# Optimization experiments

Measured on AMD Instinct MI355X. Metric: run time of the kernel, lower is better.

The kernel has to match this reference:

```python
import jax, jax.numpy as jnp
import numpy as np
import math

B, L = 32, 1000
N_CHAR, EMB, D_MODEL, N_HEADS, PRED_HS, N_OUT = 256, 512, 512, 8, 512, 8
D_HEAD = D_MODEL // N_HEADS


def _pos_encoding(seq_len, d_model, dtype=jnp.float32):
    pos = jnp.arange(seq_len, dtype=dtype)[:, None]                      # [L,1]
    div = jnp.exp(jnp.arange(0, d_model, 2, dtype=dtype) * (-math.log(10000.0) / d_model))
    pe = jnp.zeros((seq_len, d_model), dtype=dtype)
    pe = pe.at[:, 0::2].set(jnp.sin(pos * div))
    pe = pe.at[:, 1::2].set(jnp.cos(pos * div))
    return pe                                                            # [L,D]


def setup_inputs() -> dict:
    key = jax.random.key(0)
    ks = jax.random.split(key, 12)
    def xavier(k, shape):
        fan_in, fan_out = shape[1], shape[0]
        lim = math.sqrt(6.0 / (fan_in + fan_out))
        return jax.random.uniform(k, shape, jnp.float32, -lim, lim)
    data = jax.random.randint(ks[0], (B, L), 0, N_CHAR, dtype=jnp.int64)
    lengths = jnp.clip(jax.random.randint(ks[1], (B,), 0, L, dtype=jnp.int64), 1, L)
    emb = jax.random.normal(ks[2], (N_CHAR, EMB), jnp.float32) * math.sqrt(2.0 / (N_CHAR + EMB))
    return {
        'data': data,
        'lengths': lengths,
        'emb': emb,
        'Wq': xavier(ks[3], (D_MODEL, EMB)), 'bq': jnp.zeros((D_MODEL,), jnp.float32),
        'Wk': xavier(ks[4], (D_MODEL, EMB)), 'bk': jnp.zeros((D_MODEL,), jnp.float32),
        'Wv': xavier(ks[5], (D_MODEL, EMB)), 'bv': jnp.zeros((D_MODEL,), jnp.float32),
        'W1': xavier(ks[6], (PRED_HS, D_MODEL)), 'b1': jnp.full((PRED_HS,), 0.01, jnp.float32),
        'W2': xavier(ks[7], (N_OUT, PRED_HS)), 'b2': jnp.full((N_OUT,), 0.01, jnp.float32),
    }


def reference(data, lengths, emb, Wq, bq, Wk, bk, Wv, bv, W1, b1, W2, b2):
    bs, seq = data.shape
    x = emb[data]                                              # [B,L,E]
    x = x + _pos_encoding(seq, x.shape[-1], x.dtype)[None]     # positional encoding
    # q/k/v projections -> [B,L,H,dh]
    q = (x @ Wq.T + bq).reshape(bs, seq, N_HEADS, D_HEAD)
    k = (x @ Wk.T + bk).reshape(bs, seq, N_HEADS, D_HEAD)
    v = (x @ Wv.T + bv).reshape(bs, seq, N_HEADS, D_HEAD)
    scale = 1.0 / math.sqrt(D_HEAD)
    score = jnp.einsum('bqhd,bkhd->bhqk', q, k) * scale        # [B,H,L,L]
    causal = jnp.tril(jnp.ones((seq, seq), dtype=bool))        # True = keep
    score = jnp.where(causal[None, None], score, -jnp.inf)
    attn = jax.nn.softmax(score, axis=-1)
    ctx = jnp.einsum('bhqk,bkhd->bqhd', attn, v).reshape(bs, seq, D_MODEL)
    # take hidden state at last valid position per sequence
    ctx_last = jnp.take_along_axis(ctx, (lengths - 1)[:, None, None].astype(jnp.int32), axis=1)[:, 0]  # [B,D]
    h = jax.nn.leaky_relu(ctx_last @ W1.T + b1)                # pred layer 1
    out = jax.nn.relu(h @ W2.T + b2)                           # [B,8]
    out = jnp.mean(out, axis=-1)                               # [B]
    return jax.nn.leaky_relu(out)
```

## Files before the change

kernel.cpp:

```cpp
#include <hip/hip_runtime.h>
#include <math.h>

#define BATCH   32
#define LSEQ    1000
#define NHEADS  8
#define DHEAD   64
#define CHUNK   64
#define NCHUNK  16
#define PE_C    (-9.210340371976184f / 512.0f)

__device__ __forceinline__ float pe_val(int j, int e) {
  int ef = e & ~1;
  float dv  = __expf((float)ef * PE_C);
  float arg = (float)j * dv;
  return (e & 1) ? __cosf(arg) : __sinf(arg);
}

__global__ __launch_bounds__(256) void qfold_kernel(
    const int* __restrict__ data, const int* __restrict__ lengths,
    const float* __restrict__ emb,
    const float* __restrict__ Wq, const float* __restrict__ bq,
    const float* __restrict__ Wk, const float* __restrict__ bk,
    float* __restrict__ wfT4, float* __restrict__ bias_dot) {
  int h = blockIdx.x, b = blockIdx.y;
  int p = lengths[b] - 1;
  int t = threadIdx.x;
  __shared__ float xs[512];
  __shared__ float red[256];
  __shared__ float qs[64];
  int tok = data[b * LSEQ + p];
  const float* er = emb + (size_t)tok * 512;
  xs[t]       = er[t]       + pe_val(p, t);
  xs[t + 256] = er[t + 256] + pe_val(p, t + 256);
  __syncthreads();
  int col = h * 64 + (t & 63);
  int kp  = t >> 6;
  {
    const float* wr = Wq + (size_t)col * 512 + kp * 128;
    const float* xp = xs + kp * 128;
    float a = 0.0f;
    for (int e = 0; e < 128; e += 4) {
      float4 wv = *(const float4*)(wr + e);
      a += wv.x * xp[e] + wv.y * xp[e + 1] + wv.z * xp[e + 2] + wv.w * xp[e + 3];
    }
    red[t] = a;
  }
  __syncthreads();
  if (t < 64) {
    float qval = (red[t] + red[t + 64] + red[t + 128] + red[t + 192]
                  + bq[h * 64 + t]) * 0.125f;
    qs[t] = qval;
    float bd = qval * bk[h * 64 + t];
    #pragma unroll
    for (int o = 32; o > 0; o >>= 1) bd += __shfl_xor(bd, o, 64);
    if (t == 0) bias_dot[b * NHEADS + h] = bd;
  }
  __syncthreads();
  float a0 = 0.0f, a1 = 0.0f;
  const float* wkb = Wk + (size_t)(h * 64) * 512;
  for (int d = 0; d < 64; ++d) {
    float qd = qs[d];
    a0 += qd * wkb[d * 512 + t];
    a1 += qd * wkb[d * 512 + t + 256];
  }
  int bh = b * NHEADS + h;
  int e1 = t, e2 = t + 256;
  wfT4[(e1 >> 2) * 1024 + bh * 4 + (e1 & 3)] = a0;
  wfT4[(e2 >> 2) * 1024 + bh * 4 + (e2 & 3)] = a1;
}

__global__ __launch_bounds__(256) void foldmd_kernel(
    const float* __restrict__ emb, const float* __restrict__ wfT4,
    const float* __restrict__ bias_dot, float* __restrict__ MD,
    float* __restrict__ pe_tab) {
  __shared__ float rows[8 * 516];
  int t   = threadIdx.x;
  int r0  = blockIdx.x * 8;
  int bh0 = blockIdx.y * 64;
  #pragma unroll
  for (int i = 0; i < 4; ++i) {
    int fi = t + i * 256;
    int rr = fi >> 7;
    int e  = (fi & 127) * 4;
    int rg = r0 + rr;
    float4 v;
    if (rg < 256) {
      v = *(const float4*)(emb + (size_t)rg * 512 + e);
    } else {
      int j = rg - 256;
      float dv0 = __expf((float)e * PE_C);
      float dv1 = __expf((float)(e + 2) * PE_C);
      float a0 = (float)j * dv0, a1 = (float)j * dv1;
      v.x = __sinf(a0); v.y = __cosf(a0);
      v.z = __sinf(a1); v.w = __cosf(a1);
      if (blockIdx.y == 0)
        *(float4*)(pe_tab + (size_t)j * 512 + e) = v;
    }
    *(float4*)(&rows[rr * 516 + e]) = v;
  }
  __syncthreads();
  int w    = t >> 6, lane = t & 63;
  int bh   = bh0 + w * 16 + (lane & 15);
  int rp   = lane >> 4;
  const float* rw0 = rows + (2 * rp) * 516;
  const float* rw1 = rows + (2 * rp + 1) * 516;
  const float* wp  = wfT4 + (size_t)bh * 4;
  float a0 = 0.0f, a1 = 0.0f;
  #pragma unroll 8
  for (int g = 0; g < 128; ++g) {
    float4 w4 = *(const float4*)(wp + (size_t)g * 1024);
    float4 v0 = *(const float4*)(rw0 + 4 * g);
    float4 v1 = *(const float4*)(rw1 + 4 * g);
    a0 += v0.x * w4.x + v0.y * w4.y + v0.z * w4.z + v0.w * w4.w;
    a1 += v1.x * w4.x + v1.y * w4.y + v1.z * w4.z + v1.w * w4.w;
  }
  float bd = (r0 < 256) ? bias_dot[bh] : 0.0f;
  int r = r0 + 2 * rp;
  MD[(size_t)r * 256 + bh]       = a0 + bd;
  MD[(size_t)(r + 1) * 256 + bh] = a1 + bd;
}

__global__ __launch_bounds__(256) void attn_ypass_kernel(
    const int* __restrict__ data, const int* __restrict__ lengths,
    const float* __restrict__ emb, const float* __restrict__ MD,
    const float* __restrict__ pe_tab,
    float* __restrict__ mS, float* __restrict__ y_part) {
  int jc = blockIdx.x, b = blockIdx.y;
  int n = lengths[b];
  int j0 = jc * CHUNK;
  if (j0 >= n) return;
  int cnt = min(CHUNK, n - j0);
  int t = threadIdx.x;
  __shared__ float sl[CHUNK][8];
  __shared__ int   tk[CHUNK];
  __shared__ float redw[4][8];
  __shared__ float m_sh[8], s_sh[8];
  const float* Edot = MD;
  const float* Pdot = MD + 256 * 256;

  if (t < CHUNK) tk[t] = data[b * LSEQ + j0 + ((t < cnt) ? t : 0)];
  __syncthreads();

  int h = t & 7, jA = t >> 3, jB = jA + 32;
  int bh8 = b * 8 + h;
  float sA = -INFINITY, sB = -INFINITY;
  if (jA < cnt)
    sA = Edot[(size_t)tk[jA] * 256 + bh8] + Pdot[(size_t)(j0 + jA) * 256 + bh8];
  if (jB < cnt)
    sB = Edot[(size_t)tk[jB] * 256 + bh8] + Pdot[(size_t)(j0 + jB) * 256 + bh8];

  int w = t >> 6;
  float mloc = fmaxf(sA, sB);
  #pragma unroll
  for (int o = 8; o < 64; o <<= 1) mloc = fmaxf(mloc, __shfl_xor(mloc, o, 64));
  if ((t & 63) < 8) redw[w][t & 7] = mloc;
  __syncthreads();
  if (t < 8)
    m_sh[t] = fmaxf(fmaxf(redw[0][t], redw[1][t]),
                    fmaxf(redw[2][t], redw[3][t]));
  __syncthreads();
  float mh = m_sh[h];
  float pA = __expf(sA - mh);
  float pB = __expf(sB - mh);
  sl[jA][h] = pA;
  sl[jB][h] = pB;
  float sloc = pA + pB;
  #pragma unroll
  for (int o = 8; o < 64; o <<= 1) sloc += __shfl_xor(sloc, o, 64);
  if ((t & 63) < 8) redw[w][t & 7] = sloc;
  __syncthreads();
  if (t < 8) s_sh[t] = redw[0][t] + redw[1][t] + redw[2][t] + redw[3][t];

  int lane = t & 63;
  int e0i = w * 128 + lane * 2;
  float acc0[8] = {0, 0, 0, 0, 0, 0, 0, 0};
  float acc1[8] = {0, 0, 0, 0, 0, 0, 0, 0};
  const float* pe_row = pe_tab + (size_t)j0 * 512 + e0i;
  #pragma unroll 4
  for (int jj = 0; jj < cnt; ++jj) {
    int tok = tk[jj];
    float2 ev = *(const float2*)(emb + (size_t)tok * 512 + e0i);
    float2 pv = *(const float2*)(pe_row + (size_t)jj * 512);
    float x0 = ev.x + pv.x;
    float x1 = ev.y + pv.y;
    float4 pa = *(const float4*)(&sl[jj][0]);
    float4 pb = *(const float4*)(&sl[jj][4]);
    acc0[0] += pa.x * x0; acc1[0] += pa.x * x1;
    acc0[1] += pa.y * x0; acc1[1] += pa.y * x1;
    acc0[2] += pa.z * x0; acc1[2] += pa.z * x1;
    acc0[3] += pa.w * x0; acc1[3] += pa.w * x1;
    acc0[4] += pb.x * x0; acc1[4] += pb.x * x1;
    acc0[5] += pb.y * x0; acc1[5] += pb.y * x1;
    acc0[6] += pb.z * x0; acc1[6] += pb.z * x1;
    acc0[7] += pb.w * x0; acc1[7] += pb.w * x1;
  }
  size_t base = (size_t)(b * NCHUNK + jc) * 4096 + e0i;
  #pragma unroll
  for (int hh = 0; hh < 8; ++hh) {
    float2 o; o.x = acc0[hh]; o.y = acc1[hh];
    *(float2*)(y_part + base + hh * 512) = o;
  }
  if (t < 8) {
    float2 ms; ms.x = m_sh[t]; ms.y = s_sh[t];
    *(float2*)(mS + ((size_t)(b * NCHUNK + jc) * 8 + t) * 2) = ms;
  }
}

__global__ __launch_bounds__(256) void ctx_kernel(
    const int* __restrict__ lengths, const float* __restrict__ y_part,
    const float* __restrict__ mS, const float* __restrict__ Wv,
    const float* __restrict__ bv, float* __restrict__ ctx) {
  int h = blockIdx.x, b = blockIdx.y;
  int t = threadIdx.x;
  __shared__ float ys[512];
  __shared__ float red[256];
  int n = lengths[b];
  int nc = (n + CHUNK - 1) / CHUNK;
  float M = -INFINITY;
  for (int jc = 0; jc < nc; ++jc)
    M = fmaxf(M, mS[((size_t)(b * NCHUNK + jc) * 8 + h) * 2]);
  float S = 0.0f, s0 = 0.0f, s1 = 0.0f;
  for (int jc = 0; jc < nc; ++jc) {
    float2 ms = *(const float2*)(mS + ((size_t)(b * NCHUNK + jc) * 8 + h) * 2);
    float wgt = __expf(ms.x - M);
    S += wgt * ms.y;
    size_t base = (size_t)(b * NCHUNK + jc) * 4096 + h * 512;
    s0 += wgt * y_part[base + t];
    s1 += wgt * y_part[base + t + 256];
  }
  float inv = 1.0f / S;
  ys[t]       = s0 * inv;
  ys[t + 256] = s1 * inv;
  __syncthreads();
  int col = h * 64 + (t & 63);
  int kp  = t >> 6;
  const float* wr = Wv + (size_t)col * 512 + kp * 128;
  const float* xp = ys + kp * 128;
  float a = 0.0f;
  for (int e = 0; e < 128; e += 4) {
    float4 wv4 = *(const float4*)(wr + e);
    a += wv4.x * xp[e] + wv4.y * xp[e + 1] + wv4.z * xp[e + 2] + wv4.w * xp[e + 3];
  }
  red[t] = a;
  __syncthreads();
  if (t < 64)
    ctx[b * 512 + h * 64 + t] =
        red[t] + red[t + 64] + red[t + 128] + red[t + 192] + bv[h * 64 + t];
}

__global__ __launch_bounds__(256) void mlp1_kernel(
    const float* __restrict__ ctx, const float* __restrict__ W1,
    const float* __restrict__ b1, float* __restrict__ hs) {
  int chunk = blockIdx.x, b = blockIdx.y;
  int t = threadIdx.x;
  __shared__ float xs[512];
  __shared__ float red[256];
  xs[t]       = ctx[b * 512 + t];
  xs[t + 256] = ctx[b * 512 + t + 256];
  __syncthreads();
  int col = chunk * 64 + (t & 63);
  int kp  = t >> 6;
  const float* wr = W1 + (size_t)col * 512 + kp * 128;
  const float* xp = xs + kp * 128;
  float a = 0.0f;
  for (int e = 0; e < 128; e += 4) {
    float4 wv = *(const float4*)(wr + e);
    a += wv.x * xp[e] + wv.y * xp[e + 1] + wv.z * xp[e + 2] + wv.w * xp[e + 3];
  }
  red[t] = a;
  __syncthreads();
  if (t < 64) {
    float v = red[t] + red[t + 64] + red[t + 128] + red[t + 192] + b1[chunk * 64 + t];
    hs[b * 512 + chunk * 64 + t] = (v > 0.0f) ? v : 0.01f * v;
  }
}

__global__ __launch_bounds__(256) void mlp2_kernel(
    const float* __restrict__ hs, const float* __restrict__ W2,
    const float* __restrict__ b2, float* __restrict__ out) {
  int b = blockIdx.x, t = threadIdx.x;
  __shared__ float o8[8];
  int j = t >> 5, sub = t & 31;
  const float* hr  = hs + (size_t)b * 512;
  const float* w2r = W2 + (size_t)j * 512;
  float part = 0.0f;
  for (int e = sub * 16; e < sub * 16 + 16; e += 4) {
    float4 wv = *(const float4*)(w2r + e);
    float4 hv = *(const float4*)(hr + e);
    part += wv.x * hv.x + wv.y * hv.y + wv.z * hv.z + wv.w * hv.w;
  }
  #pragma unroll
  for (int o = 16; o > 0; o >>= 1) part += __shfl_xor(part, o, 64);
  if (sub == 0) o8[j] = fmaxf(part + b2[j], 0.0f);
  __syncthreads();
  if (t == 0) {
    float m = 0.0f;
    #pragma unroll
    for (int i = 0; i < 8; ++i) m += o8[i];
    m *= 0.125f;
    out[b] = (m > 0.0f) ? m : 0.01f * m;
  }
}

extern "C" void kernel_launch(void* const* d_in, const int* in_sizes, int n_in,
                              void* d_out, int out_size, void* d_ws, size_t ws_size,
                              hipStream_t stream) {
  const int*   data    = (const int*)d_in[0];
  const int*   lengths = (const int*)d_in[1];
  const float* emb     = (const float*)d_in[2];
  const float* Wq      = (const float*)d_in[3];
  const float* bq      = (const float*)d_in[4];
  const float* Wk      = (const float*)d_in[5];
  const float* bk      = (const float*)d_in[6];
  const float* Wv      = (const float*)d_in[7];
  const float* bv      = (const float*)d_in[8];
  const float* W1      = (const float*)d_in[9];
  const float* b1      = (const float*)d_in[10];
  const float* W2      = (const float*)d_in[11];
  const float* b2      = (const float*)d_in[12];
  float* out = (float*)d_out;

  char* ws = (char*)d_ws;
  float* wfT4     = (float*)(ws);
  float* MD       = (float*)(ws + 524288);
  float* bias_dot = (float*)(ws + 1810432);
  float* mS       = (float*)(ws + 1811456);
  float* y_part   = (float*)(ws + 1844224);
  float* ctx      = (float*)(ws + 10232832);
  float* hs       = (float*)(ws + 10298368);
  float* pe_tab   = (float*)(ws + 10363904);

  dim3 g1(NHEADS, BATCH);
  qfold_kernel<<<g1, 256, 0, stream>>>(data, lengths, emb, Wq, bq, Wk, bk,
                                       wfT4, bias_dot);
  dim3 g2(157, 4);
  foldmd_kernel<<<g2, 256, 0, stream>>>(emb, wfT4, bias_dot, MD, pe_tab);
  dim3 g3(NCHUNK, BATCH);
  attn_ypass_kernel<<<g3, 256, 0, stream>>>(data, lengths, emb, MD, pe_tab,
                                            mS, y_part);
  dim3 g4(NHEADS, BATCH);
  ctx_kernel<<<g4, 256, 0, stream>>>(lengths, y_part, mS, Wv, bv, ctx);
  dim3 g5(8, BATCH);
  mlp1_kernel<<<g5, 256, 0, stream>>>(ctx, W1, b1, hs);
  mlp2_kernel<<<BATCH, 256, 0, stream>>>(hs, W2, b2, out);
}
```

Baseline: 144.9 us.

## Fuse all stages into one persistent kernel with atomic grid barriers

Replaces six kernel launches with one persistent 256-block kernel that uses atomic-counter grid barriers between the query-fold, score-table, attention-pass and final MLP phases. The positional-encoding table is now written in a dedicated first phase instead of inside the score-fold stage. The final context, W1 and W2 stages are merged into one block per batch element. This removes launch gaps but adds a memset, spin barriers, and a serialized tail phase where only 32 blocks run the matrix-vector work for all heads. It also depends on all 256 blocks being co-resident to avoid deadlock.

Result: slower. 336.0 us (+131.9%).

```diff
diff --git a/kernel.cpp b/kernel.cpp
--- a/kernel.cpp
+++ b/kernel.cpp
@@ -4,9 +4,9 @@
 #define BATCH   32
 #define LSEQ    1000
 #define NHEADS  8
-#define DHEAD   64
 #define CHUNK   64
 #define NCHUNK  16
+#define NBLK    256
 #define PE_C    (-9.210340371976184f / 512.0f)
 
 __device__ __forceinline__ float pe_val(int j, int e) {
@@ -16,289 +16,299 @@
   return (e & 1) ? __cosf(arg) : __sinf(arg);
 }
 
-__global__ __launch_bounds__(256) void qfold_kernel(
+__device__ __forceinline__ void gbar(unsigned* bar, unsigned nblk) {
+  __syncthreads();
+  if (threadIdx.x == 0) {
+    __hip_atomic_fetch_add(bar, 1u, __ATOMIC_ACQ_REL, __HIP_MEMORY_SCOPE_AGENT);
+    while (__hip_atomic_load(bar, __ATOMIC_ACQUIRE, __HIP_MEMORY_SCOPE_AGENT) <
+           nblk) {
+      __builtin_amdgcn_s_sleep(2);
+    }
+  }
+  __syncthreads();
+}
+
+__global__ __launch_bounds__(256, 2) void fused_kernel(
     const int* __restrict__ data, const int* __restrict__ lengths,
     const float* __restrict__ emb,
     const float* __restrict__ Wq, const float* __restrict__ bq,
     const float* __restrict__ Wk, const float* __restrict__ bk,
-    float* __restrict__ wfT4, float* __restrict__ bias_dot) {
-  int h = blockIdx.x, b = blockIdx.y;
-  int p = lengths[b] - 1;
-  int t = threadIdx.x;
-  __shared__ float xs[512];
-  __shared__ float red[256];
-  __shared__ float qs[64];
-  int tok = data[b * LSEQ + p];
-  const float* er = emb + (size_t)tok * 512;
-  xs[t]       = er[t]       + pe_val(p, t);
-  xs[t + 256] = er[t + 256] + pe_val(p, t + 256);
-  __syncthreads();
-  int col = h * 64 + (t & 63);
-  int kp  = t >> 6;
+    const float* __restrict__ Wv, const float* __restrict__ bv,
+    const float* __restrict__ W1, const float* __restrict__ b1,
+    const float* __restrict__ W2, const float* __restrict__ b2,
+    float* __restrict__ wfT4, float* __restrict__ bias_dot,
+    float* __restrict__ MD, float* __restrict__ pe_tab,
+    float* __restrict__ mS, float* __restrict__ y_part,
+    unsigned* __restrict__ bar, float* __restrict__ out) {
+  __shared__ float smem[5400];
+  int bid = blockIdx.x;
+  int t   = threadIdx.x;
+
   {
-    const float* wr = Wq + (size_t)col * 512 + kp * 128;
-    const float* xp = xs + kp * 128;
-    float a = 0.0f;
-    for (int e = 0; e < 128; e += 4) {
-      float4 wv = *(const float4*)(wr + e);
-      a += wv.x * xp[e] + wv.y * xp[e + 1] + wv.z * xp[e + 2] + wv.w * xp[e + 3];
-    }
-    red[t] = a;
-  }
-  __syncthreads();
-  if (t < 64) {
-    float qval = (red[t] + red[t + 64] + red[t + 128] + red[t + 192]
-                  + bq[h * 64 + t]) * 0.125f;
-    qs[t] = qval;
-    float bd = qval * bk[h * 64 + t];
+    int e0 = t * 2;
+    float dvp = __expf((float)e0 * PE_C);
+    for (int j = bid; j < LSEQ; j += NBLK) {
+      float arg = (float)j * dvp;
+      float2 v;
+      v.x = __sinf(arg);
+      v.y = __cosf(arg);
+      *(float2*)(pe_tab + (size_t)j * 512 + e0) = v;
+    }
+  }
+  {
+    float* xs  = smem;
+    float* red = smem + 512;
+    float* qs  = smem + 768;
+    int h = bid & 7, b = bid >> 3;
+    int p = lengths[b] - 1;
+    int tok = data[b * LSEQ + p];
+    const float* er = emb + (size_t)tok * 512;
+    xs[t]       = er[t]       + pe_val(p, t);
+    xs[t + 256] = er[t + 256] + pe_val(p, t + 256);
+    __syncthreads();
+    int col = h * 64 + (t & 63);
+    int kp  = t >> 6;
+    {
+      const float* wr = Wq + (size_t)col * 512 + kp * 128;
+      const float* xp = xs + kp * 128;
+      float a = 0.0f;
+      for (int e = 0; e < 128; e += 4) {
+        float4 wv = *(const float4*)(wr + e);
+        a += wv.x * xp[e] + wv.y * xp[e + 1] + wv.z * xp[e + 2] + wv.w * xp[e + 3];
+      }
+      red[t] = a;
+    }
+    __syncthreads();
+    if (t < 64) {
+      float qval = (red[t] + red[t + 64] + red[t + 128] + red[t + 192]
+                    + bq[h * 64 + t]) * 0.125f;
+      qs[t] = qval;
+      float bd = qval * bk[h * 64 + t];
+      #pragma unroll
+      for (int o = 32; o > 0; o >>= 1) bd += __shfl_xor(bd, o, 64);
+      if (t == 0) bias_dot[b * NHEADS + h] = bd;
+    }
+    __syncthreads();
+    float a0 = 0.0f, a1 = 0.0f;
+    const float* wkb = Wk + (size_t)(h * 64) * 512;
+    for (int d = 0; d < 64; ++d) {
+      float qd = qs[d];
+      a0 += qd * wkb[d * 512 + t];
+      a1 += qd * wkb[d * 512 + t + 256];
+    }
+    int bh = b * NHEADS + h;
+    int e1 = t, e2 = t + 256;
+    wfT4[(e1 >> 2) * 1024 + bh * 4 + (e1 & 3)] = a0;
+    wfT4[(e2 >> 2) * 1024 + bh * 4 + (e2 & 3)] = a1;
+  }
+  gbar(bar + 0, NBLK);
+
+  {
+    float* rows = smem;
+    for (int wi = bid; wi < 628; wi += NBLK) {
+      __syncthreads();
+      int r0  = (wi % 157) * 8;
+      int bh0 = (wi / 157) * 64;
+      #pragma unroll
+      for (int i = 0; i < 4; ++i) {
+        int fi = t + i * 256;
+        int rr = fi >> 7;
+        int e  = (fi & 127) * 4;
+        int rg = r0 + rr;
+        float4 v;
+        if (rg < 256) v = *(const float4*)(emb + (size_t)rg * 512 + e);
+        else          v = *(const float4*)(pe_tab + (size_t)(rg - 256) * 512 + e);
+        *(float4*)(&rows[rr * 516 + e]) = v;
+      }
+      __syncthreads();
+      int w    = t >> 6, lane = t & 63;
+      int bh   = bh0 + w * 16 + (lane & 15);
+      int rp   = lane >> 4;
+      const float* rw0 = rows + (2 * rp) * 516;
+      const float* rw1 = rows + (2 * rp + 1) * 516;
+      const float* wp  = wfT4 + (size_t)bh * 4;
+      float a0 = 0.0f, a1 = 0.0f;
+      #pragma unroll 8
+      for (int g = 0; g < 128; ++g) {
+        float4 w4 = *(const float4*)(wp + (size_t)g * 1024);
+        float4 v0 = *(const float4*)(rw0 + 4 * g);
+        float4 v1 = *(const float4*)(rw1 + 4 * g);
+        a0 += v0.x * w4.x + v0.y * w4.y + v0.z * w4.z + v0.w * w4.w;
+        a1 += v1.x * w4.x + v1.y * w4.y + v1.z * w4.z + v1.w * w4.w;
+      }
+      float bd = (r0 < 256) ? bias_dot[bh] : 0.0f;
+      int r = r0 + 2 * rp;
+      MD[(size_t)r * 256 + bh]       = a0 + bd;
+      MD[(size_t)(r + 1) * 256 + bh] = a1 + bd;
+    }
+  }
+  gbar(bar + 1, NBLK);
+
+  for (int wi = bid; wi < 512; wi += NBLK) {
+    __syncthreads();
+    int jc = wi & 15, b = wi >> 4;
+    int n  = lengths[b];
+    int j0 = jc * CHUNK;
+    if (j0 >= n) continue;
+    int cnt = min(CHUNK, n - j0);
+    float* sl   = smem;
+    float* redw = smem + 512;
+    float* m_sh = smem + 544;
+    float* s_sh = smem + 552;
+    int*   tk   = (int*)(smem + 560);
+    const float* Edot = MD;
+    const float* Pdot = MD + 256 * 256;
+
+    if (t < CHUNK) tk[t] = data[b * LSEQ + j0 + ((t < cnt) ? t : 0)];
+    __syncthreads();
+
+    int h = t & 7, jA = t >> 3, jB = jA + 32;
+    int bh8 = b * 8 + h;
+    float sA = -INFINITY, sB = -INFINITY;
+    if (jA < cnt)
+      sA = Edot[(size_t)tk[jA] * 256 + bh8] + Pdot[(size_t)(j0 + jA) * 256 + bh8];
+    if (jB < cnt)
+      sB = Edot[(size_t)tk[jB] * 256 + bh8] + Pdot[(size_t)(j0 + jB) * 256 + bh8];
+
+    int w = t >> 6;
+    float mloc = fmaxf(sA, sB);
     #pragma unroll
-    for (int o = 32; o > 0; o >>= 1) bd += __shfl_xor(bd, o, 64);
-    if (t == 0) bias_dot[b * NHEADS + h] = bd;
-  }
-  __syncthreads();
-  float a0 = 0.0f, a1 = 0.0f;
-  const float* wkb = Wk + (size_t)(h * 64) * 512;
-  for (int d = 0; d < 64; ++d) {
-    float qd = qs[d];
-    a0 += qd * wkb[d * 512 + t];
-    a1 += qd * wkb[d * 512 + t + 256];
-  }
-  int bh = b * NHEADS + h;
-  int e1 = t, e2 = t + 256;
-  wfT4[(e1 >> 2) * 1024 + bh * 4 + (e1 & 3)] = a0;
-  wfT4[(e2 >> 2) * 1024 + bh * 4 + (e2 & 3)] = a1;
-}
-
-__global__ __launch_bounds__(256) void foldmd_kernel(
-    const float* __restrict__ emb, const float* __restrict__ wfT4,
-    const float* __restrict__ bias_dot, float* __restrict__ MD,
-    float* __restrict__ pe_tab) {
-  __shared__ float rows[8 * 516];
-  int t   = threadIdx.x;
-  int r0  = blockIdx.x * 8;
-  int bh0 = blockIdx.y * 64;
-  #pragma unroll
-  for (int i = 0; i < 4; ++i) {
-    int fi = t + i * 256;
-    int rr = fi >> 7;
-    int e  = (fi & 127) * 4;
-    int rg = r0 + rr;
-    float4 v;
-    if (rg < 256) {
-      v = *(const float4*)(emb + (size_t)rg * 512 + e);
-    } else {
-      int j = rg - 256;
-      float dv0 = __expf((float)e * PE_C);
-      float dv1 = __expf((float)(e + 2) * PE_C);
-      float a0 = (float)j * dv0, a1 = (float)j * dv1;
-      v.x = __sinf(a0); v.y = __cosf(a0);
-      v.z = __sinf(a1); v.w = __cosf(a1);
-      if (blockIdx.y == 0)
-        *(float4*)(pe_tab + (size_t)j * 512 + e) = v;
-    }
-    *(float4*)(&rows[rr * 516 + e]) = v;
-  }
-  __syncthreads();
-  int w    = t >> 6, lane = t & 63;
-  int bh   = bh0 + w * 16 + (lane & 15);
-  int rp   = lane >> 4;
-  const float* rw0 = rows + (2 * rp) * 516;
-  const float* rw1 = rows + (2 * rp + 1) * 516;
-  const float* wp  = wfT4 + (size_t)bh * 4;
-  float a0 = 0.0f, a1 = 0.0f;
-  #pragma unroll 8
-  for (int g = 0; g < 128; ++g) {
-    float4 w4 = *(const float4*)(wp + (size_t)g * 1024);
-    float4 v0 = *(const float4*)(rw0 + 4 * g);
-    float4 v1 = *(const float4*)(rw1 + 4 * g);
-    a0 += v0.x * w4.x + v0.y * w4.y + v0.z * w4.z + v0.w * w4.w;
-    a1 += v1.x * w4.x + v1.y * w4.y + v1.z * w4.z + v1.w * w4.w;
-  }
-  float bd = (r0 < 256) ? bias_dot[bh] : 0.0f;
-  int r = r0 + 2 * rp;
-  MD[(size_t)r * 256 + bh]       = a0 + bd;
-  MD[(size_t)(r + 1) * 256 + bh] = a1 + bd;
-}
-
-__global__ __launch_bounds__(256) void attn_ypass_kernel(
-    const int* __restrict__ data, const int* __restrict__ lengths,
-    const float* __restrict__ emb, const float* __restrict__ MD,
-    const float* __restrict__ pe_tab,
-    float* __restrict__ mS, float* __restrict__ y_part) {
-  int jc = blockIdx.x, b = blockIdx.y;
-  int n = lengths[b];
-  int j0 = jc * CHUNK;
-  if (j0 >= n) return;
-  int cnt = min(CHUNK, n - j0);
-  int t = threadIdx.x;
-  __shared__ float sl[CHUNK][8];
-  __shared__ int   tk[CHUNK];
-  __shared__ float redw[4][8];
-  __shared__ float m_sh[8], s_sh[8];
-  const float* Edot = MD;
-  const float* Pdot = MD + 256 * 256;
-
-  if (t < CHUNK) tk[t] = data[b * LSEQ + j0 + ((t < cnt) ? t : 0)];
-  __syncthreads();
-
-  int h = t & 7, jA = t >> 3, jB = jA + 32;
-  int bh8 = b * 8 + h;
-  float sA = -INFINITY, sB = -INFINITY;
-  if (jA < cnt)
-    sA = Edot[(size_t)tk[jA] * 256 + bh8] + Pdot[(size_t)(j0 + jA) * 256 + bh8];
-  if (jB < cnt)
-    sB = Edot[(size_t)tk[jB] * 256 + bh8] + Pdot[(size_t)(j0 + jB) * 256 + bh8];
-
-  int w = t >> 6;
-  float mloc = fmaxf(sA, sB);
-  #pragma unroll
-  for (int o = 8; o < 64; o <<= 1) mloc = fmaxf(mloc, __shfl_xor(mloc, o, 64));
-  if ((t & 63) < 8) redw[w][t & 7] = mloc;
-  __syncthreads();
-  if (t < 8)
-    m_sh[t] = fmaxf(fmaxf(redw[0][t], redw[1][t]),
-                    fmaxf(redw[2][t], redw[3][t]));
-  __syncthreads();
-  float mh = m_sh[h];
-  float pA = __expf(sA - mh);
-  float pB = __expf(sB - mh);
-  sl[jA][h] = pA;
-  sl[jB][h] = pB;
-  float sloc = pA + pB;
-  #pragma unroll
-  for (int o = 8; o < 64; o <<= 1) sloc += __shfl_xor(sloc, o, 64);
-  if ((t & 63) < 8) redw[w][t & 7] = sloc;
-  __syncthreads();
-  if (t < 8) s_sh[t] = redw[0][t] + redw[1][t] + redw[2][t] + redw[3][t];
-
-  int lane = t & 63;
-  int e0i = w * 128 + lane * 2;
-  float acc0[8] = {0, 0, 0, 0, 0, 0, 0, 0};
-  float acc1[8] = {0, 0, 0, 0, 0, 0, 0, 0};
-  const float* pe_row = pe_tab + (size_t)j0 * 512 + e0i;
-  #pragma unroll 4
-  for (int jj = 0; jj < cnt; ++jj) {
-    int tok = tk[jj];
-    float2 ev = *(const float2*)(emb + (size_t)tok * 512 + e0i);
-    float2 pv = *(const float2*)(pe_row + (size_t)jj * 512);
-    float x0 = ev.x + pv.x;
-    float x1 = ev.y + pv.y;
-    float4 pa = *(const float4*)(&sl[jj][0]);
-    float4 pb = *(const float4*)(&sl[jj][4]);
-    acc0[0] += pa.x * x0; acc1[0] += pa.x * x1;
-    acc0[1] += pa.y * x0; acc1[1] += pa.y * x1;
-    acc0[2] += pa.z * x0; acc1[2] += pa.z * x1;
-    acc0[3] += pa.w * x0; acc1[3] += pa.w * x1;
-    acc0[4] += pb.x * x0; acc1[4] += pb.x * x1;
-    acc0[5] += pb.y * x0; acc1[5] += pb.y * x1;
-    acc0[6] += pb.z * x0; acc1[6] += pb.z * x1;
-    acc0[7] += pb.w * x0; acc1[7] += pb.w * x1;
-  }
-  size_t base = (size_t)(b * NCHUNK + jc) * 4096 + e0i;
-  #pragma unroll
-  for (int hh = 0; hh < 8; ++hh) {
-    float2 o; o.x = acc0[hh]; o.y = acc1[hh];
-    *(float2*)(y_part + base + hh * 512) = o;
-  }
-  if (t < 8) {
-    float2 ms; ms.x = m_sh[t]; ms.y = s_sh[t];
-    *(float2*)(mS + ((size_t)(b * NCHUNK + jc) * 8 + t) * 2) = ms;
-  }
-}
-
-__global__ __launch_bounds__(256) void ctx_kernel(
-    const int* __restrict__ lengths, const float* __restrict__ y_part,
-    const float* __restrict__ mS, const float* __restrict__ Wv,
-    const float* __restrict__ bv, float* __restrict__ ctx) {
-  int h = blockIdx.x, b = blockIdx.y;
-  int t = threadIdx.x;
-  __shared__ float ys[512];
-  __shared__ float red[256];
-  int n = lengths[b];
-  int nc = (n + CHUNK - 1) / CHUNK;
-  float M = -INFINITY;
-  for (int jc = 0; jc < nc; ++jc)
-    M = fmaxf(M, mS[((size_t)(b * NCHUNK + jc) * 8 + h) * 2]);
-  float S = 0.0f, s0 = 0.0f, s1 = 0.0f;
-  for (int jc = 0; jc < nc; ++jc) {
-    float2 ms = *(const float2*)(mS + ((size_t)(b * NCHUNK + jc) * 8 + h) * 2);
-    float wgt = __expf(ms.x - M);
-    S += wgt * ms.y;
-    size_t base = (size_t)(b * NCHUNK + jc) * 4096 + h * 512;
-    s0 += wgt * y_part[base + t];
-    s1 += wgt * y_part[base + t + 256];
-  }
-  float inv = 1.0f / S;
-  ys[t]       = s0 * inv;
-  ys[t + 256] = s1 * inv;
-  __syncthreads();
-  int col = h * 64 + (t & 63);
-  int kp  = t >> 6;
-  const float* wr = Wv + (size_t)col * 512 + kp * 128;
-  const float* xp = ys + kp * 128;
-  float a = 0.0f;
-  for (int e = 0; e < 128; e += 4) {
-    float4 wv4 = *(const float4*)(wr + e);
-    a += wv4.x * xp[e] + wv4.y * xp[e + 1] + wv4.z * xp[e + 2] + wv4.w * xp[e + 3];
-  }
-  red[t] = a;
-  __syncthreads();
-  if (t < 64)
-    ctx[b * 512 + h * 64 + t] =
-        red[t] + red[t + 64] + red[t + 128] + red[t + 192] + bv[h * 64 + t];
-}
-
-__global__ __launch_bounds__(256) void mlp1_kernel(
-    const float* __restrict__ ctx, const float* __restrict__ W1,
-    const float* __restrict__ b1, float* __restrict__ hs) {
-  int chunk = blockIdx.x, b = blockIdx.y;
-  int t = threadIdx.x;
-  __shared__ float xs[512];
-  __shared__ float red[256];
-  xs[t]       = ctx[b * 512 + t];
-  xs[t + 256] = ctx[b * 512 + t + 256];
-  __syncthreads();
-  int col = chunk * 64 + (t & 63);
-  int kp  = t >> 6;
-  const float* wr = W1 + (size_t)col * 512 + kp * 128;
-  const float* xp = xs + kp * 128;
-  float a = 0.0f;
-  for (int e = 0; e < 128; e += 4) {
-    float4 wv = *(const float4*)(wr + e);
-    a += wv.x * xp[e] + wv.y * xp[e + 1] + wv.z * xp[e + 2] + wv.w * xp[e + 3];
-  }
-  red[t] = a;
-  __syncthreads();
-  if (t < 64) {
-    float v = red[t] + red[t + 64] + red[t + 128] + red[t + 192] + b1[chunk * 64 + t];
-    hs[b * 512 + chunk * 64 + t] = (v > 0.0f) ? v : 0.01f * v;
-  }
-}
-
-__global__ __launch_bounds__(256) void mlp2_kernel(
-    const float* __restrict__ hs, const float* __restrict__ W2,
-    const float* __restrict__ b2, float* __restrict__ out) {
-  int b = blockIdx.x, t = threadIdx.x;
-  __shared__ float o8[8];
-  int j = t >> 5, sub = t & 31;
-  const float* hr  = hs + (size_t)b * 512;
-  const float* w2r = W2 + (size_t)j * 512;
-  float part = 0.0f;
-  for (int e = sub * 16; e < sub * 16 + 16; e += 4) {
-    float4 wv = *(const float4*)(w2r + e);
-    float4 hv = *(const float4*)(hr + e);
-    part += wv.x * hv.x + wv.y * hv.y + wv.z * hv.z + wv.w * hv.w;
-  }
-  #pragma unroll
-  for (int o = 16; o > 0; o >>= 1) part += __shfl_xor(part, o, 64);
-  if (sub == 0) o8[j] = fmaxf(part + b2[j], 0.0f);
-  __syncthreads();
-  if (t == 0) {
-    float m = 0.0f;
+    for (int o = 8; o < 64; o <<= 1) mloc = fmaxf(mloc, __shfl_xor(mloc, o, 64));
+    if ((t & 63) < 8) redw[w * 8 + (t & 7)] = mloc;
+    __syncthreads();
+    if (t < 8)
+      m_sh[t] = fmaxf(fmaxf(redw[t], redw[8 + t]),
+                      fmaxf(redw[16 + t], redw[24 + t]));
+    __syncthreads();
+    float mh = m_sh[h];
+    float pA = __expf(sA - mh);
+    float pB = __expf(sB - mh);
+    sl[jA * 8 + h] = pA;
+    sl[jB * 8 + h] = pB;
+    float sloc = pA + pB;
     #pragma unroll
-    for (int i = 0; i < 8; ++i) m += o8[i];
-    m *= 0.125f;
-    out[b] = (m > 0.0f) ? m : 0.01f * m;
+    for (int o = 8; o < 64; o <<= 1) sloc += __shfl_xor(sloc, o, 64);
+    if ((t & 63) < 8) redw[w * 8 + (t & 7)] = sloc;
+    __syncthreads();
+    if (t < 8) s_sh[t] = redw[t] + redw[8 + t] + redw[16 + t] + redw[24 + t];
+
+    int lane = t & 63;
+    int e0i = w * 128 + lane * 2;
+    float acc0[8] = {0, 0, 0, 0, 0, 0, 0, 0};
+    float acc1[8] = {0, 0, 0, 0, 0, 0, 0, 0};
+    const float* pe_row = pe_tab + (size_t)j0 * 512 + e0i;
+    #pragma unroll 4
+    for (int jj = 0; jj < cnt; ++jj) {
+      int tok = tk[jj];
+      float2 ev = *(const float2*)(emb + (size_t)tok * 512 + e0i);
+      float2 pv = *(const float2*)(pe_row + (size_t)jj * 512);
+      float x0 = ev.x + pv.x;
+      float x1 = ev.y + pv.y;
+      float4 pa = *(const float4*)(&sl[jj * 8]);
+      float4 pb = *(const float4*)(&sl[jj * 8 + 4]);
+      acc0[0] += pa.x * x0; acc1[0] += pa.x * x1;
+      acc0[1] += pa.y * x0; acc1[1] += pa.y * x1;
+      acc0[2] += pa.z * x0; acc1[2] += pa.z * x1;
+      acc0[3] += pa.w * x0; acc1[3] += pa.w * x1;
+      acc0[4] += pb.x * x0; acc1[4] += pb.x * x1;
+      acc0[5] += pb.y * x0; acc1[5] += pb.y * x1;
+      acc0[6] += pb.z * x0; acc1[6] += pb.z * x1;
+      acc0[7] += pb.w * x0; acc1[7] += pb.w * x1;
+    }
+    size_t base = (size_t)(b * NCHUNK + jc) * 4096 + e0i;
+    #pragma unroll
+    for (int hh = 0; hh < 8; ++hh) {
+      float2 o; o.x = acc0[hh]; o.y = acc1[hh];
+      *(float2*)(y_part + base + hh * 512) = o;
+    }
+    if (t < 8) {
+      float2 ms; ms.x = m_sh[t]; ms.y = s_sh[t];
+      *(float2*)(mS + ((size_t)(b * NCHUNK + jc) * 8 + t) * 2) = ms;
+    }
+  }
+  gbar(bar + 2, NBLK);
+
+  if (bid < BATCH) {
+    int b = bid;
+    float* ysh   = smem;
+    float* red   = smem + 4096;
+    float* ctx_s = smem + 4352;
+    float* hs_s  = smem + 4864;
+    float* o8    = smem + 5376;
+    int n  = lengths[b];
+    int nc = (n + CHUNK - 1) / CHUNK;
+    for (int h = 0; h < 8; ++h) {
+      float M = -INFINITY;
+      for (int jc = 0; jc < nc; ++jc)
+        M = fmaxf(M, mS[((size_t)(b * NCHUNK + jc) * 8 + h) * 2]);
+      float S = 0.0f, s0 = 0.0f, s1 = 0.0f;
+      for (int jc = 0; jc < nc; ++jc) {
+        float2 ms = *(const float2*)(mS + ((size_t)(b * NCHUNK + jc) * 8 + h) * 2);
+        float wgt = __expf(ms.x - M);
+        S += wgt * ms.y;
+        size_t base = (size_t)(b * NCHUNK + jc) * 4096 + h * 512;
+        s0 += wgt * y_part[base + t];
+        s1 += wgt * y_part[base + t + 256];
+      }
+      float inv = 1.0f / S;
+      ysh[h * 512 + t]       = s0 * inv;
+      ysh[h * 512 + t + 256] = s1 * inv;
+    }
+    __syncthreads();
+    for (int h = 0; h < 8; ++h) {
+      int col = h * 64 + (t & 63);
+      int kp  = t >> 6;
+      const float* wr = Wv + (size_t)col * 512 + kp * 128;
+      const float* xp = ysh + h * 512 + kp * 128;
+      float a = 0.0f;
+      for (int e = 0; e < 128; e += 4) {
+        float4 wv4 = *(const float4*)(wr + e);
+        a += wv4.x * xp[e] + wv4.y * xp[e + 1] + wv4.z * xp[e + 2] + wv4.w * xp[e + 3];
+      }
+      red[t] = a;
+      __syncthreads();
+      if (t < 64)
+        ctx_s[h * 64 + t] =
+            red[t] + red[t + 64] + red[t + 128] + red[t + 192] + bv[h * 64 + t];
+      __syncthreads();
+    }
+    for (int ch = 0; ch < 8; ++ch) {
+      int col = ch * 64 + (t & 63);
+      int kp  = t >> 6;
+      const float* wr = W1 + (size_t)col * 512 + kp * 128;
+      const float* xp = ctx_s + kp * 128;
+      float a = 0.0f;
+      for (int e = 0; e < 128; e += 4) {
+        float4 wv = *(const float4*)(wr + e);
+        a += wv.x * xp[e] + wv.y * xp[e + 1] + wv.z * xp[e + 2] + wv.w * xp[e + 3];
+      }
+      red[t] = a;
+      __syncthreads();
+      if (t < 64) {
+        float v = red[t] + red[t + 64] + red[t + 128] + red[t + 192] + b1[ch * 64 + t];
+        hs_s[ch * 64 + t] = (v > 0.0f) ? v : 0.01f * v;
+      }
+      __syncthreads();
+    }
+    int j = t >> 5, sub = t & 31;
+    const float* w2r = W2 + (size_t)j * 512;
+    float part = 0.0f;
+    for (int e = sub * 16; e < sub * 16 + 16; e += 4) {
+      float4 wv = *(const float4*)(w2r + e);
+      float4 hv = *(const float4*)(hs_s + e);
+      part += wv.x * hv.x + wv.y * hv.y + wv.z * hv.z + wv.w * hv.w;
+    }
+    #pragma unroll
+    for (int o = 16; o > 0; o >>= 1) part += __shfl_xor(part, o, 64);
+    if (sub == 0) o8[j] = fmaxf(part + b2[j], 0.0f);
+    __syncthreads();
+    if (t == 0) {
+      float m = 0.0f;
+      #pragma unroll
+      for (int i = 0; i < 8; ++i) m += o8[i];
+      m *= 0.125f;
+      out[b] = (m > 0.0f) ? m : 0.01f * m;
+    }
   }
 }
 
@@ -321,26 +331,17 @@
   float* out = (float*)d_out;
 
   char* ws = (char*)d_ws;
-  float* wfT4     = (float*)(ws);
-  float* MD       = (float*)(ws + 524288);
-  float* bias_dot = (float*)(ws + 1810432);
-  float* mS       = (float*)(ws + 1811456);
-  float* y_part   = (float*)(ws + 1844224);
-  float* ctx      = (float*)(ws + 10232832);
-  float* hs       = (float*)(ws + 10298368);
-  float* pe_tab   = (float*)(ws + 10363904);
-
-  dim3 g1(NHEADS, BATCH);
-  qfold_kernel<<<g1, 256, 0, stream>>>(data, lengths, emb, Wq, bq, Wk, bk,
-                                       wfT4, bias_dot);
-  dim3 g2(157, 4);
-  foldmd_kernel<<<g2, 256, 0, stream>>>(emb, wfT4, bias_dot, MD, pe_tab);
-  dim3 g3(NCHUNK, BATCH);
-  attn_ypass_kernel<<<g3, 256, 0, stream>>>(data, lengths, emb, MD, pe_tab,
-                                            mS, y_part);
-  dim3 g4(NHEADS, BATCH);
-  ctx_kernel<<<g4, 256, 0, stream>>>(lengths, y_part, mS, Wv, bv, ctx);
-  dim3 g5(8, BATCH);
-  mlp1_kernel<<<g5, 256, 0, stream>>>(ctx, W1, b1, hs);
-  mlp2_kernel<<<BATCH, 256, 0, stream>>>(hs, W2, b2, out);
+  float*    wfT4     = (float*)(ws);
+  float*    MD       = (float*)(ws + 524288);
+  float*    bias_dot = (float*)(ws + 1810432);
+  float*    mS       = (float*)(ws + 1811456);
+  float*    y_part   = (float*)(ws + 1844224);
+  float*    pe_tab   = (float*)(ws + 10363904);
+  unsigned* bar      = (unsigned*)(ws + 12411904);
+
+  hipMemsetAsync(bar, 0, 64, stream);
+
+  fused_kernel<<<dim3(NBLK), dim3(256), 0, stream>>>(
+      data, lengths, emb, Wq, bq, Wk, bk, Wv, bv, W1, b1, W2, b2,
+      wfT4, bias_dot, MD, pe_tab, mS, y_part, bar, out);
 }
```

## Fuse ctx and MLP tail kernels and move PE table build into qfold

Applied to the files above, without the earlier changes.

Merges the ctx, mlp1 and mlp2 kernels into one tail kernel with one block per batch element, keeping ctx and hidden activations in shared memory. This removes two launches and their global round trips. The positional-encoding table is now built in qfold_kernel, so foldmd_kernel only loads it instead of computing sin/cos. The cost is that the tail runs on only 32 blocks, each looping serially over heads and chunks, which reduces parallelism for the Wv and W1 GEMVs.

Measured after the change: 225.9 us. 55.9% more time.

```diff
diff --git a/kernel.cpp b/kernel.cpp
--- a/kernel.cpp
+++ b/kernel.cpp
@@ -4,7 +4,6 @@
 #define BATCH   32
 #define LSEQ    1000
 #define NHEADS  8
-#define DHEAD   64
 #define CHUNK   64
 #define NCHUNK  16
 #define PE_C    (-9.210340371976184f / 512.0f)
@@ -21,8 +20,10 @@
     const float* __restrict__ emb,
     const float* __restrict__ Wq, const float* __restrict__ bq,
     const float* __restrict__ Wk, const float* __restrict__ bk,
-    float* __restrict__ wfT4, float* __restrict__ bias_dot) {
+    float* __restrict__ wfT4, float* __restrict__ bias_dot,
+    float* __restrict__ pe_tab) {
   int h = blockIdx.x, b = blockIdx.y;
+  int bid = b * NHEADS + h;
   int p = lengths[b] - 1;
   int t = threadIdx.x;
   __shared__ float xs[512];
@@ -67,12 +68,21 @@
   int e1 = t, e2 = t + 256;
   wfT4[(e1 >> 2) * 1024 + bh * 4 + (e1 & 3)] = a0;
   wfT4[(e2 >> 2) * 1024 + bh * 4 + (e2 & 3)] = a1;
+  int e0 = t * 2;
+  float dvp = __expf((float)e0 * PE_C);
+  for (int j = bid; j < LSEQ; j += 256) {
+    float arg = (float)j * dvp;
+    float2 v;
+    v.x = __sinf(arg);
+    v.y = __cosf(arg);
+    *(float2*)(pe_tab + (size_t)j * 512 + e0) = v;
+  }
 }
 
 __global__ __launch_bounds__(256) void foldmd_kernel(
-    const float* __restrict__ emb, const float* __restrict__ wfT4,
-    const float* __restrict__ bias_dot, float* __restrict__ MD,
-    float* __restrict__ pe_tab) {
+    const float* __restrict__ emb, const float* __restrict__ pe_tab,
+    const float* __restrict__ wfT4, const float* __restrict__ bias_dot,
+    float* __restrict__ MD) {
   __shared__ float rows[8 * 516];
   int t   = threadIdx.x;
   int r0  = blockIdx.x * 8;
@@ -84,18 +94,8 @@
     int e  = (fi & 127) * 4;
     int rg = r0 + rr;
     float4 v;
-    if (rg < 256) {
-      v = *(const float4*)(emb + (size_t)rg * 512 + e);
-    } else {
-      int j = rg - 256;
-      float dv0 = __expf((float)e * PE_C);
-      float dv1 = __expf((float)(e + 2) * PE_C);
-      float a0 = (float)j * dv0, a1 = (float)j * dv1;
-      v.x = __sinf(a0); v.y = __cosf(a0);
-      v.z = __sinf(a1); v.w = __cosf(a1);
-      if (blockIdx.y == 0)
-        *(float4*)(pe_tab + (size_t)j * 512 + e) = v;
-    }
+    if (rg < 256) v = *(const float4*)(emb + (size_t)rg * 512 + e);
+    else          v = *(const float4*)(pe_tab + (size_t)(rg - 256) * 512 + e);
     *(float4*)(&rows[rr * 516 + e]) = v;
   }
   __syncthreads();
@@ -206,87 +206,80 @@
   }
 }
 
-__global__ __launch_bounds__(256) void ctx_kernel(
+__global__ __launch_bounds__(256) void tail_kernel(
     const int* __restrict__ lengths, const float* __restrict__ y_part,
     const float* __restrict__ mS, const float* __restrict__ Wv,
-    const float* __restrict__ bv, float* __restrict__ ctx) {
-  int h = blockIdx.x, b = blockIdx.y;
+    const float* __restrict__ bv, const float* __restrict__ W1,
+    const float* __restrict__ b1, const float* __restrict__ W2,
+    const float* __restrict__ b2, float* __restrict__ out) {
+  __shared__ float ysh[8 * 512];
+  __shared__ float red[256];
+  __shared__ float ctx_s[512];
+  __shared__ float hs_s[512];
+  __shared__ float o8[8];
+  int b = blockIdx.x;
   int t = threadIdx.x;
-  __shared__ float ys[512];
-  __shared__ float red[256];
-  int n = lengths[b];
+  int n  = lengths[b];
   int nc = (n + CHUNK - 1) / CHUNK;
-  float M = -INFINITY;
-  for (int jc = 0; jc < nc; ++jc)
-    M = fmaxf(M, mS[((size_t)(b * NCHUNK + jc) * 8 + h) * 2]);
-  float S = 0.0f, s0 = 0.0f, s1 = 0.0f;
-  for (int jc = 0; jc < nc; ++jc) {
-    float2 ms = *(const float2*)(mS + ((size_t)(b * NCHUNK + jc) * 8 + h) * 2);
-    float wgt = __expf(ms.x - M);
-    S += wgt * ms.y;
-    size_t base = (size_t)(b * NCHUNK + jc) * 4096 + h * 512;
-    s0 += wgt * y_part[base + t];
-    s1 += wgt * y_part[base + t + 256];
-  }
-  float inv = 1.0f / S;
-  ys[t]       = s0 * inv;
-  ys[t + 256] = s1 * inv;
-  __syncthreads();
-  int col = h * 64 + (t & 63);
-  int kp  = t >> 6;
-  const float* wr = Wv + (size_t)col * 512 + kp * 128;
-  const float* xp = ys + kp * 128;
-  float a = 0.0f;
-  for (int e = 0; e < 128; e += 4) {
-    float4 wv4 = *(const float4*)(wr + e);
-    a += wv4.x * xp[e] + wv4.y * xp[e + 1] + wv4.z * xp[e + 2] + wv4.w * xp[e + 3];
-  }
-  red[t] = a;
-  __syncthreads();
-  if (t < 64)
-    ctx[b * 512 + h * 64 + t] =
-        red[t] + red[t + 64] + red[t + 128] + red[t + 192] + bv[h * 64 + t];
-}
-
-__global__ __launch_bounds__(256) void mlp1_kernel(
-    const float* __restrict__ ctx, const float* __restrict__ W1,
-    const float* __restrict__ b1, float* __restrict__ hs) {
-  int chunk = blockIdx.x, b = blockIdx.y;
-  int t = threadIdx.x;
-  __shared__ float xs[512];
-  __shared__ float red[256];
-  xs[t]       = ctx[b * 512 + t];
-  xs[t + 256] = ctx[b * 512 + t + 256];
-  __syncthreads();
-  int col = chunk * 64 + (t & 63);
-  int kp  = t >> 6;
-  const float* wr = W1 + (size_t)col * 512 + kp * 128;
-  const float* xp = xs + kp * 128;
-  float a = 0.0f;
-  for (int e = 0; e < 128; e += 4) {
-    float4 wv = *(const float4*)(wr + e);
-    a += wv.x * xp[e] + wv.y * xp[e + 1] + wv.z * xp[e + 2] + wv.w * xp[e + 3];
-  }
-  red[t] = a;
-  __syncthreads();
-  if (t < 64) {
-    float v = red[t] + red[t + 64] + red[t + 128] + red[t + 192] + b1[chunk * 64 + t];
-    hs[b * 512 + chunk * 64 + t] = (v > 0.0f) ? v : 0.01f * v;
-  }
-}
-
-__global__ __launch_bounds__(256) void mlp2_kernel(
-    const float* __restrict__ hs, const float* __restrict__ W2,
-    const float* __restrict__ b2, float* __restrict__ out) {
-  int b = blockIdx.x, t = threadIdx.x;
-  __shared__ float o8[8];
+  for (int h = 0; h < 8; ++h) {
+    float M = -INFINITY;
+    for (int jc = 0; jc < nc; ++jc)
+      M = fmaxf(M, mS[((size_t)(b * NCHUNK + jc) * 8 + h) * 2]);
+    float S = 0.0f, s0 = 0.0f, s1 = 0.0f;
+    for (int jc = 0; jc < nc; ++jc) {
+      float2 ms = *(const float2*)(mS + ((size_t)(b * NCHUNK + jc) * 8 + h) * 2);
+      float wgt = __expf(ms.x - M);
+      S += wgt * ms.y;
+      size_t base = (size_t)(b * NCHUNK + jc) * 4096 + h * 512;
+      s0 += wgt * y_part[base + t];
+      s1 += wgt * y_part[base + t + 256];
+    }
+    float inv = 1.0f / S;
+    ysh[h * 512 + t]       = s0 * inv;
+    ysh[h * 512 + t + 256] = s1 * inv;
+  }
+  __syncthreads();
+  for (int h = 0; h < 8; ++h) {
+    int col = h * 64 + (t & 63);
+    int kp  = t >> 6;
+    const float* wr = Wv + (size_t)col * 512 + kp * 128;
+    const float* xp = ysh + h * 512 + kp * 128;
+    float a = 0.0f;
+    for (int e = 0; e < 128; e += 4) {
+      float4 wv4 = *(const float4*)(wr + e);
+      a += wv4.x * xp[e] + wv4.y * xp[e + 1] + wv4.z * xp[e + 2] + wv4.w * xp[e + 3];
+    }
+    red[t] = a;
+    __syncthreads();
+    if (t < 64)
+      ctx_s[h * 64 + t] =
+          red[t] + red[t + 64] + red[t + 128] + red[t + 192] + bv[h * 64 + t];
+    __syncthreads();
+  }
+  for (int ch = 0; ch < 8; ++ch) {
+    int col = ch * 64 + (t & 63);
+    int kp  = t >> 6;
+    const float* wr = W1 + (size_t)col * 512 + kp * 128;
+    const float* xp = ctx_s + kp * 128;
+    float a = 0.0f;
+    for (int e = 0; e < 128; e += 4) {
+      float4 wv = *(const float4*)(wr + e);
+      a += wv.x * xp[e] + wv.y * xp[e + 1] + wv.z * xp[e + 2] + wv.w * xp[e + 3];
+    }
+    red[t] = a;
+    __syncthreads();
+    if (t < 64) {
+      float v = red[t] + red[t + 64] + red[t + 128] + red[t + 192] + b1[ch * 64 + t];
+      hs_s[ch * 64 + t] = (v > 0.0f) ? v : 0.01f * v;
+    }
+    __syncthreads();
+  }
   int j = t >> 5, sub = t & 31;
-  const float* hr  = hs + (size_t)b * 512;
   const float* w2r = W2 + (size_t)j * 512;
   float part = 0.0f;
   for (int e = sub * 16; e < sub * 16 + 16; e += 4) {
     float4 wv = *(const float4*)(w2r + e);
-    float4 hv = *(const float4*)(hr + e);
+    float4 hv = *(const float4*)(hs_s + e);
     part += wv.x * hv.x + wv.y * hv.y + wv.z * hv.z + wv.w * hv.w;
   }
   #pragma unroll
@@ -326,21 +319,16 @@
   float* bias_dot = (float*)(ws + 1810432);
   float* mS       = (float*)(ws + 1811456);
   float* y_part   = (float*)(ws + 1844224);
-  float* ctx      = (float*)(ws + 10232832);
-  float* hs       = (float*)(ws + 10298368);
-  float* pe_tab   = (float*)(ws + 10363904);
+  float* pe_tab   = (float*)(ws + 10232832);
 
   dim3 g1(NHEADS, BATCH);
   qfold_kernel<<<g1, 256, 0, stream>>>(data, lengths, emb, Wq, bq, Wk, bk,
-                                       wfT4, bias_dot);
+                                       wfT4, bias_dot, pe_tab);
   dim3 g2(157, 4);
-  foldmd_kernel<<<g2, 256, 0, stream>>>(emb, wfT4, bias_dot, MD, pe_tab);
+  foldmd_kernel<<<g2, 256, 0, stream>>>(emb, pe_tab, wfT4, bias_dot, MD);
   dim3 g3(NCHUNK, BATCH);
   attn_ypass_kernel<<<g3, 256, 0, stream>>>(data, lengths, emb, MD, pe_tab,
                                             mS, y_part);
-  dim3 g4(NHEADS, BATCH);
-  ctx_kernel<<<g4, 256, 0, stream>>>(lengths, y_part, mS, Wv, bv, ctx);
-  dim3 g5(8, BATCH);
-  mlp1_kernel<<<g5, 256, 0, stream>>>(ctx, W1, b1, hs);
-  mlp2_kernel<<<BATCH, 256, 0, stream>>>(hs, W2, b2, out);
-}
+  tail_kernel<<<BATCH, 256, 0, stream>>>(lengths, y_part, mS, Wv, bv,
+                                         W1, b1, W2, b2, out);
+}
```
